# Performance work log

Measured on AMD Instinct MI355X. Metric: run time of the kernel, lower is better.

The kernel has to match this reference:

```python
import jax, jax.numpy as jnp
import numpy as np

B, C, H, W = 8, 3, 512, 512


def _spd(key, shape_prefix, c):
    a = jax.random.normal(key, shape_prefix + (c, c), dtype=jnp.float32)
    return a @ jnp.swapaxes(a, -1, -2) + jnp.eye(c, dtype=jnp.float32)


def setup_inputs() -> dict:
    key = jax.random.key(0)
    k1, k2, k3, k4, k5 = jax.random.split(key, 5)
    target = jax.random.normal(k1, (B, C, H, W), dtype=jnp.float32)
    mu = jax.random.normal(k2, (B, C, H, W), dtype=jnp.float32)
    # per-pixel covariance matrices; sigma_y must be SPD for inverse/log-det
    sigma_mu = _spd(k3, (B, H, W), C)
    sigma_n = _spd(k4, (B, H, W), C)
    sigma_y = _spd(k5, (B, H, W), C)
    return {"target": target, "mu": mu, "sigma_mu": sigma_mu,
            "sigma_n": sigma_n, "sigma_y": sigma_y}


def reference(target, mu, sigma_mu, sigma_n, sigma_y):
    # T: residual per pixel, channels-last  [B,H,W,C]
    T = jnp.transpose(target - mu, (0, 2, 3, 1))
    inv = jnp.linalg.inv(sigma_y)                      # [B,H,W,C,C] tiny 3x3 batched inverse
    # quadratic form 0.5 * T^t Sigma^{-1} T            [B,H,W]
    t1 = 0.5 * jnp.einsum('bhwc,bhwcd,bhwd->bhw', T, inv, T)
    t2 = 0.5 * jnp.log(jnp.linalg.det(sigma_y))        # [B,H,W]
    loss = jnp.mean(t1 + t2)
    # torch code zeroes loss if quadratic term blows up
    loss = jnp.where(jnp.max(t1) > 1e8, jnp.zeros_like(loss), loss)
    return loss
```

## Files before the change

### kernel.cpp

```cpp
#include <hip/hip_runtime.h>

constexpr int Cc = 3;
constexpr int HW = 512 * 512;
constexpr int NPIX = 8 * HW;
constexpr int TPB  = 128;
constexpr int TILE_PX = 512;
constexpr int NTILE = NPIX / TILE_PX;
constexpr int TPBLK = 4;
constexpr int NBLK = NTILE / TPBLK;

constexpr int T4  = TILE_PX * 3 / 4;
constexpr int S4  = TILE_PX * 9 / 4;
constexpr int BUF4 = 2 * T4 + S4;


__global__ __launch_bounds__(TPB, 1) void map_loss_main(
    const float* __restrict__ target,
    const float* __restrict__ mu,
    const float* __restrict__ sigma_y,
    double* __restrict__ part_sum,
    float* __restrict__ part_max)
{
    __shared__ float4 lds[2 * BUF4];
    __shared__ double ssum[2];
    __shared__ float  smax[2];

    const int tid = threadIdx.x;
    const int bid = blockIdx.x;

    double local_sum = 0.0;
    float local_max = 0.0f;

    auto stage = [&](int g, int bufsel) {
        float4* bb = &lds[bufsel * BUF4];
        const long long px0 = (long long)g * TILE_PX;
        const int b  = (int)(px0 >> 18);
        const int hw = (int)px0 & (HW - 1);
        const long long cbase = (long long)b * (Cc * HW) + hw;
        const float4* tsrc = (const float4*)(target + cbase);
        const float4* msrc = (const float4*)(mu + cbase);
        #pragma unroll
        for (int k = 0; k < 3; ++k) {
            const int j = k * TPB + tid;
            __builtin_amdgcn_global_load_lds(
                (const __attribute__((address_space(1))) void*)(tsrc + k * (HW / 4) + tid),
                (__attribute__((address_space(3))) void*)(bb + j), 16, 0, 0);
            __builtin_amdgcn_global_load_lds(
                (const __attribute__((address_space(1))) void*)(msrc + k * (HW / 4) + tid),
                (__attribute__((address_space(3))) void*)(bb + T4 + j), 16, 0, 0);
        }
        const float4* ssrc = (const float4*)sigma_y + (long long)g * S4;
        #pragma unroll
        for (int k = 0; k < 9; ++k) {
            const int s = k * TPB + tid;
            const int c = (s >> 6) & 7;
            __builtin_amdgcn_global_load_lds(
                (const __attribute__((address_space(1))) void*)(ssrc + (s ^ c)),
                (__attribute__((address_space(3))) void*)(bb + 2 * T4 + s), 16, 0, 0);
        }
    };

    auto compute = [&](int bufsel) {
        const float4* bb = &lds[bufsel * BUF4];
        float4 d0 = bb[0 * TPB + tid];
        float4 d1 = bb[1 * TPB + tid];
        float4 d2 = bb[2 * TPB + tid];
        const float4 m0 = bb[T4 + 0 * TPB + tid];
        const float4 m1 = bb[T4 + 1 * TPB + tid];
        const float4 m2 = bb[T4 + 2 * TPB + tid];
        d0.x -= m0.x; d0.y -= m0.y; d0.z -= m0.z; d0.w -= m0.w;
        d1.x -= m1.x; d1.y -= m1.y; d1.z -= m1.z; d1.w -= m1.w;
        d2.x -= m2.x; d2.y -= m2.y; d2.z -= m2.z; d2.w -= m2.w;

        union { float4 v[9]; float f[36]; } S;
        #pragma unroll
        for (int m = 0; m < 9; ++m) {
            const int r = 9 * tid + m;
            const int x = r ^ ((r >> 6) & 7);
            S.v[m] = bb[2 * T4 + x];
        }

        const float Tv0[4] = {d0.x, d0.y, d0.z, d0.w};
        const float Tv1[4] = {d1.x, d1.y, d1.z, d1.w};
        const float Tv2[4] = {d2.x, d2.y, d2.z, d2.w};

        #pragma unroll
        for (int i = 0; i < 4; ++i) {
            const float* s = S.f + i * 9;
            float s00 = s[0], s01 = s[1], s02 = s[2];
            float s11 = s[4], s12 = s[5], s22 = s[8];

            float a00 = s11 * s22 - s12 * s12;
            float a01 = s02 * s12 - s01 * s22;
            float a02 = s01 * s12 - s02 * s11;
            float a11 = s00 * s22 - s02 * s02;
            float a12 = s01 * s02 - s00 * s12;
            float a22 = s00 * s11 - s01 * s01;

            float det = s00 * a00 + s01 * a01 + s02 * a02;

            float t0 = Tv0[i], t1 = Tv1[i], t2 = Tv2[i];
            float quad = t0 * t0 * a00 + t1 * t1 * a11 + t2 * t2 * a22
                       + 2.0f * (t0 * t1 * a01 + t0 * t2 * a02 + t1 * t2 * a12);

            float t1term = 0.5f * quad / det;
            float t2term = 0.5f * logf(det);

            local_sum += (double)(t1term + t2term);
            local_max = fmaxf(local_max, t1term);
        }
    };

    const int g0 = bid * TPBLK;

    stage(g0 + 0, 0);
    stage(g0 + 1, 1);

    asm volatile("s_waitcnt vmcnt(15)" ::: "memory");
    __builtin_amdgcn_s_barrier();
    __builtin_amdgcn_sched_barrier(0);
    compute(0);
    __builtin_amdgcn_s_barrier();
    stage(g0 + 2, 0);

    asm volatile("s_waitcnt vmcnt(15)" ::: "memory");
    __builtin_amdgcn_s_barrier();
    __builtin_amdgcn_sched_barrier(0);
    compute(1);
    __builtin_amdgcn_s_barrier();
    stage(g0 + 3, 1);

    asm volatile("s_waitcnt vmcnt(15)" ::: "memory");
    __builtin_amdgcn_s_barrier();
    __builtin_amdgcn_sched_barrier(0);
    compute(0);
    __builtin_amdgcn_s_barrier();

    asm volatile("s_waitcnt vmcnt(0)" ::: "memory");
    __builtin_amdgcn_s_barrier();
    __builtin_amdgcn_sched_barrier(0);
    compute(1);

    for (int off = 32; off > 0; off >>= 1) {
        local_sum += __shfl_down(local_sum, off, 64);
        local_max = fmaxf(local_max, __shfl_down(local_max, off, 64));
    }
    const int w = tid >> 6;
    const int lane = tid & 63;
    if (lane == 0) { ssum[w] = local_sum; smax[w] = local_max; }
    __syncthreads();

    if (tid == 0) {
        part_sum[bid] = ssum[0] + ssum[1];
        part_max[bid] = fmaxf(smax[0], smax[1]);
    }
}

__global__ __launch_bounds__(256) void map_loss_finalize(
    const double* __restrict__ part_sum,
    const float* __restrict__ part_max,
    float* __restrict__ out)
{
    double s = 0.0;
    float m = 0.0f;
    for (int i = threadIdx.x; i < NBLK; i += 256) {
        s += part_sum[i];
        m = fmaxf(m, part_max[i]);
    }

    for (int off = 32; off > 0; off >>= 1) {
        s += __shfl_down(s, off, 64);
        m = fmaxf(m, __shfl_down(m, off, 64));
    }

    __shared__ double ssum[4];
    __shared__ float  smax[4];
    int wave = threadIdx.x >> 6;
    int lane = threadIdx.x & 63;
    if (lane == 0) { ssum[wave] = s; smax[wave] = m; }
    __syncthreads();

    if (threadIdx.x == 0) {
        double bs = ssum[0] + ssum[1] + ssum[2] + ssum[3];
        float  bm = fmaxf(fmaxf(smax[0], smax[1]), fmaxf(smax[2], smax[3]));
        out[0] = (bm > 1e8f) ? 0.0f : (float)(bs / (double)NPIX);
    }
}

extern "C" void kernel_launch(void* const* d_in, const int* in_sizes, int n_in,
                              void* d_out, int out_size, void* d_ws, size_t ws_size,
                              hipStream_t stream) {
    const float* target  = (const float*)d_in[0];
    const float* mu      = (const float*)d_in[1];
    const float* sigma_y = (const float*)d_in[4];
    float* out = (float*)d_out;

    double* part_sum = (double*)d_ws;
    float*  part_max = (float*)((char*)d_ws + NBLK * sizeof(double));

    map_loss_main<<<NBLK, TPB, 0, stream>>>(target, mu, sigma_y, part_sum, part_max);
    map_loss_finalize<<<1, 256, 0, stream>>>(part_sum, part_max, out);
}
```

Baseline: 217.6 us.

## Use single-wave blocks to drop barriers and LDS swizzle in pipelined loss kernel

Blocks shrink from two waves to one wave of 64 threads, with 256-pixel tiles and eight tiles per block. Because each block is now a single wave, the s_barrier calls and the shared-memory cross-wave reduction go away. The double-buffered staging loop is written as an unrolled loop that waits on lgkmcnt before reusing a buffer, and the XOR swizzle on the sigma LDS layout is dropped. The aim is to remove barrier stalls and raise occupancy, since launch_bounds no longer pins one block per SIMD. The risk is that the unswizzled stride-9 float4 LDS reads may cause more bank conflicts.

```diff
diff --git a/kernel.cpp b/kernel.cpp
--- a/kernel.cpp
+++ b/kernel.cpp
@@ -3,18 +3,19 @@
 constexpr int Cc = 3;
 constexpr int HW = 512 * 512;
 constexpr int NPIX = 8 * HW;
-constexpr int TPB  = 128;
-constexpr int TILE_PX = 512;
+constexpr int TPB  = 64;
+constexpr int TILE_PX = 256;
 constexpr int NTILE = NPIX / TILE_PX;
-constexpr int TPBLK = 4;
+constexpr int TPBLK = 8;
 constexpr int NBLK = NTILE / TPBLK;
 
-constexpr int T4  = TILE_PX * 3 / 4;
-constexpr int S4  = TILE_PX * 9 / 4;
+constexpr int TM4  = TILE_PX / 4;
+constexpr int T4   = 3 * TM4;
+constexpr int S4   = TILE_PX * 9 / 4;
 constexpr int BUF4 = 2 * T4 + S4;
 
 
-__global__ __launch_bounds__(TPB, 1) void map_loss_main(
+__global__ __launch_bounds__(TPB) void map_loss_main(
     const float* __restrict__ target,
     const float* __restrict__ mu,
     const float* __restrict__ sigma_y,
@@ -22,8 +23,6 @@
     float* __restrict__ part_max)
 {
     __shared__ float4 lds[2 * BUF4];
-    __shared__ double ssum[2];
-    __shared__ float  smax[2];
 
     const int tid = threadIdx.x;
     const int bid = blockIdx.x;
@@ -36,49 +35,42 @@
         const long long px0 = (long long)g * TILE_PX;
         const int b  = (int)(px0 >> 18);
         const int hw = (int)px0 & (HW - 1);
-        const long long cbase = (long long)b * (Cc * HW) + hw;
-        const float4* tsrc = (const float4*)(target + cbase);
-        const float4* msrc = (const float4*)(mu + cbase);
+        const long long cbase4 = ((long long)b * (Cc * HW) + hw) >> 2;
+        const float4* tsrc = (const float4*)target + cbase4;
+        const float4* msrc = (const float4*)mu + cbase4;
         #pragma unroll
         for (int k = 0; k < 3; ++k) {
-            const int j = k * TPB + tid;
             __builtin_amdgcn_global_load_lds(
                 (const __attribute__((address_space(1))) void*)(tsrc + k * (HW / 4) + tid),
-                (__attribute__((address_space(3))) void*)(bb + j), 16, 0, 0);
+                (__attribute__((address_space(3))) void*)(bb + k * 64), 16, 0, 0);
             __builtin_amdgcn_global_load_lds(
                 (const __attribute__((address_space(1))) void*)(msrc + k * (HW / 4) + tid),
-                (__attribute__((address_space(3))) void*)(bb + T4 + j), 16, 0, 0);
+                (__attribute__((address_space(3))) void*)(bb + T4 + k * 64), 16, 0, 0);
         }
         const float4* ssrc = (const float4*)sigma_y + (long long)g * S4;
         #pragma unroll
         for (int k = 0; k < 9; ++k) {
-            const int s = k * TPB + tid;
-            const int c = (s >> 6) & 7;
             __builtin_amdgcn_global_load_lds(
-                (const __attribute__((address_space(1))) void*)(ssrc + (s ^ c)),
-                (__attribute__((address_space(3))) void*)(bb + 2 * T4 + s), 16, 0, 0);
+                (const __attribute__((address_space(1))) void*)(ssrc + k * 64 + tid),
+                (__attribute__((address_space(3))) void*)(bb + 2 * T4 + k * 64), 16, 0, 0);
         }
     };
 
     auto compute = [&](int bufsel) {
         const float4* bb = &lds[bufsel * BUF4];
-        float4 d0 = bb[0 * TPB + tid];
-        float4 d1 = bb[1 * TPB + tid];
-        float4 d2 = bb[2 * TPB + tid];
-        const float4 m0 = bb[T4 + 0 * TPB + tid];
-        const float4 m1 = bb[T4 + 1 * TPB + tid];
-        const float4 m2 = bb[T4 + 2 * TPB + tid];
+        float4 d0 = bb[0 * 64 + tid];
+        float4 d1 = bb[1 * 64 + tid];
+        float4 d2 = bb[2 * 64 + tid];
+        const float4 m0 = bb[T4 + 0 * 64 + tid];
+        const float4 m1 = bb[T4 + 1 * 64 + tid];
+        const float4 m2 = bb[T4 + 2 * 64 + tid];
         d0.x -= m0.x; d0.y -= m0.y; d0.z -= m0.z; d0.w -= m0.w;
         d1.x -= m1.x; d1.y -= m1.y; d1.z -= m1.z; d1.w -= m1.w;
         d2.x -= m2.x; d2.y -= m2.y; d2.z -= m2.z; d2.w -= m2.w;
 
         union { float4 v[9]; float f[36]; } S;
         #pragma unroll
-        for (int m = 0; m < 9; ++m) {
-            const int r = 9 * tid + m;
-            const int x = r ^ ((r >> 6) & 7);
-            S.v[m] = bb[2 * T4 + x];
-        }
+        for (int k = 0; k < 9; ++k) S.v[k] = bb[2 * T4 + 9 * tid + k];
 
         const float Tv0[4] = {d0.x, d0.y, d0.z, d0.w};
         const float Tv1[4] = {d1.x, d1.y, d1.z, d1.w};
@@ -116,43 +108,29 @@
     stage(g0 + 0, 0);
     stage(g0 + 1, 1);
 
-    asm volatile("s_waitcnt vmcnt(15)" ::: "memory");
-    __builtin_amdgcn_s_barrier();
-    __builtin_amdgcn_sched_barrier(0);
-    compute(0);
-    __builtin_amdgcn_s_barrier();
-    stage(g0 + 2, 0);
-
-    asm volatile("s_waitcnt vmcnt(15)" ::: "memory");
-    __builtin_amdgcn_s_barrier();
-    __builtin_amdgcn_sched_barrier(0);
-    compute(1);
-    __builtin_amdgcn_s_barrier();
-    stage(g0 + 3, 1);
-
-    asm volatile("s_waitcnt vmcnt(15)" ::: "memory");
-    __builtin_amdgcn_s_barrier();
-    __builtin_amdgcn_sched_barrier(0);
-    compute(0);
-    __builtin_amdgcn_s_barrier();
-
-    asm volatile("s_waitcnt vmcnt(0)" ::: "memory");
-    __builtin_amdgcn_s_barrier();
-    __builtin_amdgcn_sched_barrier(0);
-    compute(1);
+    #pragma unroll
+    for (int i = 0; i < TPBLK; ++i) {
+        if (i < TPBLK - 1) {
+            asm volatile("s_waitcnt vmcnt(15)" ::: "memory");
+        } else {
+            asm volatile("s_waitcnt vmcnt(0)" ::: "memory");
+        }
+        __builtin_amdgcn_sched_barrier(0);
+        compute(i & 1);
+        if (i + 2 < TPBLK) {
+            asm volatile("s_waitcnt lgkmcnt(0)" ::: "memory");
+            __builtin_amdgcn_sched_barrier(0);
+            stage(g0 + i + 2, i & 1);
+        }
+    }
 
     for (int off = 32; off > 0; off >>= 1) {
         local_sum += __shfl_down(local_sum, off, 64);
         local_max = fmaxf(local_max, __shfl_down(local_max, off, 64));
     }
-    const int w = tid >> 6;
-    const int lane = tid & 63;
-    if (lane == 0) { ssum[w] = local_sum; smax[w] = local_max; }
-    __syncthreads();
-
     if (tid == 0) {
-        part_sum[bid] = ssum[0] + ssum[1];
-        part_max[bid] = fmaxf(smax[0], smax[1]);
+        part_sum[bid] = local_sum;
+        part_max[bid] = local_max;
     }
 }
 
```

New measurement: 218.0 us. Within noise of the previous version (+0.2%).
